# Kernel tuning notes

Hardware: AMD Instinct MI355X
Metric: run time of the kernel (lower is better)

The kernel has to match this reference:

```python
import jax, jax.numpy as jnp
import numpy as np
from jax import lax

_DN = ('NCHW', 'OIHW', 'NCHW')


def _box1(s, k):
    # Separable box sum (all-ones kxk kernel) on a single-channel map (B,1,H,W).
    pad = (k - 1) // 2
    kh = jnp.ones((1, 1, k, 1), s.dtype)
    kw = jnp.ones((1, 1, 1, k), s.dtype)
    y = lax.conv_general_dilated(s, kh, (1, 1), [(pad, pad), (0, 0)], dimension_numbers=_DN)
    return lax.conv_general_dilated(y, kw, (1, 1), [(0, 0), (pad, pad)], dimension_numbers=_DN)


def _cgf(x, y, k, eps):
    # ConvGuidedFilterDlicate with weight-1 Conv2d(C,C,k): every output channel of
    # box_filter(t) equals box_sum(t.sum(channels)), so we keep channel dim = 1 and broadcast.
    B, C, H, W = x.shape
    Nc = C * _box1(jnp.ones((1, 1, H, W), x.dtype), k)           # box_filter(ones(1,C,H,W))
    mean_x = _box1(x.sum(1, keepdims=True), k) / Nc              # (B,1,H,W)
    mean_y = _box1(y.sum(1, keepdims=True), k) / Nc
    cov_xy = _box1((x * y).sum(1, keepdims=True), k) / Nc - mean_x * mean_y
    var_x = _box1((x * x).sum(1, keepdims=True), k) / Nc - mean_x * mean_x
    A = cov_xy / (var_x + eps)
    b = mean_y - A * mean_x
    # torch's A/b have C identical channels; box_filter then sums them -> factor C.
    mean_A = C * _box1(A, k)
    mean_b = C * _box1(b, k)
    return mean_A * y + mean_b                                   # broadcasts to (B,C,H,W)


def setup_inputs() -> dict:
    key = jax.random.key(0)
    k1, k2 = jax.random.split(key)
    x_hr = jax.random.normal(k1, (16, 3, 512, 512), jnp.float32)
    w1 = jax.random.normal(k2, (3, 9), jnp.float32) * 0.1        # conv1 weight (O, 3*nin1)
    return {"x_hr": x_hr, "w1": w1}


def reference(x_hr, w1):
    F1 = _cgf(x_hr, x_hr, 3, 0.16)
    F2 = _cgf(F1, F1, 7, 0.04)
    F3 = _cgf(F2, F2, 15, 0.01)
    D = jnp.concatenate([x_hr - F1, F1 - F2, F2 - F3], axis=1)   # (B,9,H,W)
    return jnp.einsum('oi,bihw->bohw', w1, D)                    # 1x1 conv, no bias
```

## Files before the change

kernel.cpp:

```cpp
#include <hip/hip_runtime.h>

#define BB 16
#define CC 3
#define HH 512
#define WW 512
#define HWP (HH*WW)
#define NMAP ((size_t)BB*HWP)

template <int P, int CH, int MODE>
__global__ __launch_bounds__(512, (MODE == 3 ? 2 : 4))
void stage(const float* __restrict__ xin, const float2* __restrict__ sqin,
           float2* __restrict__ abo, float2* __restrict__ sqo,
           const float2* __restrict__ ab1, const float2* __restrict__ ab2,
           const float* __restrict__ w1, float* __restrict__ outp, float eps)
{
    constexpr int RD  = 2*P + 1;
    constexpr int LW  = 512 + 2*P;
    constexpr int NCH = HH / CH;
    __shared__ float2 eA[LW];
    __shared__ float2 eB[LW];

    const int t  = threadIdx.x;
    const int bx = blockIdx.x;
    const int b  = bx / NCH;
    const int h0 = (bx % NCH) * CH;
    const size_t mapbase = (size_t)b * HWP;
    const float*  xb  = (MODE != 2) ? (xin + (size_t)b * CC * HWP) : nullptr;
    const float2* sqb = (MODE != 1) ? (sqin + mapbase) : nullptr;

    if (t < 2*P) {
        int sl = (t < P) ? t : (512 + t);
        eA[sl] = make_float2(0.f, 0.f);
        eB[sl] = make_float2(0.f, 0.f);
    }

    const int w   = t;
    const int wlo = (w - P < 0) ? 0 : w - P;
    const int whi = (w + P > WW-1) ? WW-1 : w + P;
    const float rcw = 1.0f / (float)(whi - wlo + 1);

    float cs0 = 0.f, cs1 = 0.f;
    float ca  = 0.f, cb  = 0.f;
    float rA[RD], rB[RD];

    auto loadSQ = [&](int rr, float& sv, float& qv) {
        size_t o = (size_t)rr * WW + w;
        if constexpr (MODE == 1) {
            float x0 = xb[o], x1 = xb[o + HWP], x2 = xb[o + 2*HWP];
            sv = x0 + x1 + x2;
            qv = x0*x0 + x1*x1 + x2*x2;
        } else {
            float2 v = sqb[o];
            sv = v.x; qv = v.y;
        }
    };

    auto advance = [&](int r) {
        int rin = r + P, rout = r - P - 1;
        if (rin < HH)  { float sv, qv; loadSQ(rin,  sv, qv); cs0 += sv; cs1 += qv; }
        if (rout >= 0) { float sv, qv; loadSQ(rout, sv, qv); cs0 -= sv; cs1 -= qv; }
    };

    auto phase1 = [&](int r, float& Aout, float& Bout) {
        eA[t + P] = make_float2(cs0, cs1);
        __syncthreads();
        float hs0 = 0.f, hs1 = 0.f;
#pragma unroll
        for (int d = 0; d <= 2*P; ++d) { float2 v = eA[t + d]; hs0 += v.x; hs1 += v.y; }
        __syncthreads();
        int rlo = (r - P < 0) ? 0 : r - P;
        int rhi = (r + P > HH-1) ? HH-1 : r + P;
        float rNc  = (1.f/3.f) * rcw / (float)(rhi - rlo + 1);
        float mean = hs0 * rNc;
        float var  = hs1 * rNc - mean * mean;
        float A    = var / (var + eps);
        Aout = A;
        Bout = mean * (1.f - A);
    };

    float w1r[27];
    if constexpr (MODE == 3) {
#pragma unroll
        for (int k = 0; k < 27; ++k) w1r[k] = w1[k];
    }

#pragma unroll
    for (int d = 0; d <= 2*P; ++d) {
        int rr = h0 - 2*P + d;
        if (rr >= 0) { float sv, qv; loadSQ(rr, sv, qv); cs0 += sv; cs1 += qv; }
    }

#pragma unroll
    for (int j = 0; j < 2*P; ++j) {
        int r = h0 - P + j;
        if (j > 0) advance(r);
        float A = 0.f, Bv = 0.f;
        if (r >= 0) { phase1(r, A, Bv); ca += A; cb += Bv; }
        rA[j % RD] = A; rB[j % RD] = Bv;
    }

#pragma unroll
    for (int i = 0; i < CH; ++i) {
        int r = h0 + P + i;
        int h = h0 + i;
        advance(r);
        float A = 0.f, Bv = 0.f;
        if (r < HH) { phase1(r, A, Bv); ca += A; cb += Bv; }
        rA[(2*P + i) % RD] = A; rB[(2*P + i) % RD] = Bv;

        eB[t + P] = make_float2(ca, cb);
        __syncthreads();
        float sA = 0.f, sB = 0.f;
#pragma unroll
        for (int d = 0; d <= 2*P; ++d) { float2 v = eB[t + d]; sA += v.x; sB += v.y; }
        __syncthreads();

        size_t oi = mapbase + (size_t)h * WW + w;
        if constexpr (MODE != 3) {
            abo[oi] = make_float2(sA, sB);
            float sv, qv; loadSQ(h, sv, qv);
            float mA = 3.f * sA, mb = 3.f * sB;
            sqo[oi] = make_float2(mA*sv + 3.f*mb,
                                  mA*mA*qv + 2.f*mA*mb*sv + 3.f*mb*mb);
        } else {
            float a3 = 3.f*sA, b3 = 3.f*sB;
            float2 v1 = ab1[oi], v2 = ab2[oi];
            float a1 = 3.f*v1.x, b1 = 3.f*v1.y;
            float a2 = 3.f*v2.x, b2 = 3.f*v2.y;
            float P1 = a1,      Q1 = b1;
            float P2 = a2 * P1, Q2 = a2 * Q1 + b2;
            float P3 = a3 * P2, Q3 = a3 * Q2 + b3;
            float alpha[3] = {1.f - P1, P1 - P2, P2 - P3};
            float beta[3]  = {-Q1,      Q1 - Q2, Q2 - Q3};
            size_t xo = (size_t)h * WW + w;
            float xv0 = xb[xo], xv1 = xb[xo + HWP], xv2 = xb[xo + 2*HWP];
#pragma unroll
            for (int o = 0; o < 3; ++o) {
                float acc = 0.f;
#pragma unroll
                for (int g = 0; g < 3; ++g) {
                    float w0v = w1r[o*9 + g*3 + 0];
                    float wv1 = w1r[o*9 + g*3 + 1];
                    float w2v = w1r[o*9 + g*3 + 2];
                    acc += alpha[g] * (w0v*xv0 + wv1*xv1 + w2v*xv2)
                         + beta[g]  * (w0v + wv1 + w2v);
                }
                outp[(size_t)b * CC * HWP + (size_t)o * HWP + xo] = acc;
            }
        }
        ca -= rA[i % RD]; cb -= rB[i % RD];
    }
}

extern "C" void kernel_launch(void* const* d_in, const int* in_sizes, int n_in,
                              void* d_out, int out_size, void* d_ws, size_t ws_size,
                              hipStream_t stream) {
    (void)in_sizes; (void)n_in; (void)out_size; (void)ws_size;
    const float* x  = (const float*)d_in[0];
    const float* w1 = (const float*)d_in[1];
    float* out = (float*)d_out;

    float2* sq1 = (float2*)d_ws;
    float2* sq2 = sq1 + NMAP;
    float2* ab1 = sq2 + NMAP;
    float2* ab2 = ab1 + NMAP;

    dim3 bl(512);
    dim3 g(BB * (HH / 16));

    stage<1,16,1><<<g, bl, 0, stream>>>(x, nullptr, ab1, sq1,
                                        nullptr, nullptr, nullptr, nullptr, 0.16f);
    stage<3,16,2><<<g, bl, 0, stream>>>(nullptr, sq1, ab2, sq2,
                                        nullptr, nullptr, nullptr, nullptr, 0.04f);
    stage<7,16,3><<<g, bl, 0, stream>>>(x, sq2, nullptr, nullptr,
                                        ab1, ab2, w1, out, 0.01f);
}
```

Before: 220.7 us.

## Rewrite guided-filter stages with two-column threads and fused single-barrier row pipeline

```diff
diff --git a/kernel.cpp b/kernel.cpp
--- a/kernel.cpp
+++ b/kernel.cpp
@@ -1,154 +1,199 @@
 #include <hip/hip_runtime.h>
 
 #define BB 16
-#define CC 3
 #define HH 512
 #define WW 512
 #define HWP (HH*WW)
 #define NMAP ((size_t)BB*HWP)
 
+struct __align__(16) V4 { float x, y, z, w; };
+__device__ __forceinline__ V4 v4(float a, float b, float c, float d) { V4 r; r.x=a; r.y=b; r.z=c; r.w=d; return r; }
+__device__ __forceinline__ V4 v4z() { return v4(0.f,0.f,0.f,0.f); }
+__device__ __forceinline__ V4 vadd(V4 a, V4 b) { return v4(a.x+b.x, a.y+b.y, a.z+b.z, a.w+b.w); }
+__device__ __forceinline__ V4 vsub(V4 a, V4 b) { return v4(a.x-b.x, a.y-b.y, a.z-b.z, a.w-b.w); }
+
 template <int P, int CH, int MODE>
-__global__ __launch_bounds__(512, (MODE == 3 ? 2 : 4))
+__global__ __launch_bounds__(256, 2)
 void stage(const float* __restrict__ xin, const float2* __restrict__ sqin,
            float2* __restrict__ abo, float2* __restrict__ sqo,
-           const float2* __restrict__ ab1, const float2* __restrict__ ab2,
-           const float* __restrict__ w1, float* __restrict__ outp, float eps)
+           const float2* __restrict__ abp1, const float2* __restrict__ abp2,
+           const float* __restrict__ wt, float* __restrict__ outp, float eps)
 {
+    constexpr int PH  = (P - 1) / 2;
     constexpr int RD  = 2*P + 1;
-    constexpr int LW  = 512 + 2*P;
+    constexpr int NIT = CH + 2*P + 1;
     constexpr int NCH = HH / CH;
-    __shared__ float2 eA[LW];
-    __shared__ float2 eB[LW];
+    constexpr int NWG = BB * NCH;
+    constexpr int NPS = 256 + 2*PH;
+    constexpr int NEV = 257 + PH;
+    constexpr int NOD = 258 + PH;
+
+    __shared__ V4 PS[2][NPS];
+    __shared__ V4 EV[2][NEV];
+    __shared__ V4 OD[2][NOD];
 
     const int t  = threadIdx.x;
-    const int bx = blockIdx.x;
-    const int b  = bx / NCH;
-    const int h0 = (bx % NCH) * CH;
-    const size_t mapbase = (size_t)b * HWP;
-    const float*  xb  = (MODE != 2) ? (xin + (size_t)b * CC * HWP) : nullptr;
-    const float2* sqb = (MODE != 1) ? (sqin + mapbase) : nullptr;
-
-    if (t < 2*P) {
-        int sl = (t < P) ? t : (512 + t);
-        eA[sl] = make_float2(0.f, 0.f);
-        eB[sl] = make_float2(0.f, 0.f);
-    }
-
-    const int w   = t;
-    const int wlo = (w - P < 0) ? 0 : w - P;
-    const int whi = (w + P > WW-1) ? WW-1 : w + P;
-    const float rcw = 1.0f / (float)(whi - wlo + 1);
-
-    float cs0 = 0.f, cs1 = 0.f;
-    float ca  = 0.f, cb  = 0.f;
-    float rA[RD], rB[RD];
-
-    auto loadSQ = [&](int rr, float& sv, float& qv) {
-        size_t o = (size_t)rr * WW + w;
+    int bx = blockIdx.x;
+    int bid = (bx & 7) * (NWG / 8) + (bx >> 3);
+    const int b  = bid / NCH;
+    const int h0 = (bid % NCH) * CH;
+    const size_t mb_ = (size_t)b * HWP;
+    const float*  xb  = (MODE != 2) ? (xin + (size_t)b * 3 * HWP) : nullptr;
+    const float2* sqb = (MODE != 1) ? (sqin + mb_) : nullptr;
+
+    if (t < PH) {
+        PS[0][t] = v4z(); PS[1][t] = v4z();
+        PS[0][256+PH+t] = v4z(); PS[1][256+PH+t] = v4z();
+    }
+    if (t < PH + 1) {
+        OD[0][t] = v4z(); OD[1][t] = v4z();
+        EV[0][256+t] = v4z(); EV[1][256+t] = v4z();
+    }
+
+    const int c0 = 2*t, c1 = c0 + 1;
+    auto cwf = [&](int c) -> float {
+        int lo = c - P < 0 ? 0 : c - P, hi = c + P > WW-1 ? WW-1 : c + P;
+        return (float)(hi - lo + 1);
+    };
+    const float cw0 = cwf(c0), cw1 = cwf(c1);
+
+    auto loadrow = [&](int rr) -> V4 {
         if constexpr (MODE == 1) {
-            float x0 = xb[o], x1 = xb[o + HWP], x2 = xb[o + 2*HWP];
-            sv = x0 + x1 + x2;
-            qv = x0*x0 + x1*x1 + x2*x2;
+            size_t o = (size_t)rr * WW + c0;
+            float2 a0 = *(const float2*)(xb + o);
+            float2 a1 = *(const float2*)(xb + o + HWP);
+            float2 a2 = *(const float2*)(xb + o + 2*HWP);
+            return v4(a0.x+a1.x+a2.x, a0.x*a0.x + a1.x*a1.x + a2.x*a2.x,
+                      a0.y+a1.y+a2.y, a0.y*a0.y + a1.y*a1.y + a2.y*a2.y);
         } else {
-            float2 v = sqb[o];
-            sv = v.x; qv = v.y;
+            float4 v = ((const float4*)(sqb + (size_t)rr * WW))[t];
+            return v4(v.x, v.y, v.z, v.w);
         }
     };
 
-    auto advance = [&](int r) {
-        int rin = r + P, rout = r - P - 1;
-        if (rin < HH)  { float sv, qv; loadSQ(rin,  sv, qv); cs0 += sv; cs1 += qv; }
-        if (rout >= 0) { float sv, qv; loadSQ(rout, sv, qv); cs0 -= sv; cs1 -= qv; }
-    };
-
-    auto phase1 = [&](int r, float& Aout, float& Bout) {
-        eA[t + P] = make_float2(cs0, cs1);
-        __syncthreads();
-        float hs0 = 0.f, hs1 = 0.f;
-#pragma unroll
-        for (int d = 0; d <= 2*P; ++d) { float2 v = eA[t + d]; hs0 += v.x; hs1 += v.y; }
-        __syncthreads();
-        int rlo = (r - P < 0) ? 0 : r - P;
-        int rhi = (r + P > HH-1) ? HH-1 : r + P;
-        float rNc  = (1.f/3.f) * rcw / (float)(rhi - rlo + 1);
-        float mean = hs0 * rNc;
-        float var  = hs1 * rNc - mean * mean;
-        float A    = var / (var + eps);
-        Aout = A;
-        Bout = mean * (1.f - A);
-    };
+    V4 csv = v4z(), cav = v4z();
+    V4 rgv[RD];
+#pragma unroll
+    for (int i = 0; i < RD; ++i) rgv[i] = v4z();
+
+#pragma unroll
+    for (int d = 0; d <= 2*P; ++d) {
+        int rr = h0 - 2*P + d;
+        if (rr >= 0) csv = vadd(csv, loadrow(rr));
+    }
+    V4 nin = loadrow(h0 + 1);
 
     float w1r[27];
     if constexpr (MODE == 3) {
 #pragma unroll
-        for (int k = 0; k < 27; ++k) w1r[k] = w1[k];
-    }
-
-#pragma unroll
-    for (int d = 0; d <= 2*P; ++d) {
-        int rr = h0 - 2*P + d;
-        if (rr >= 0) { float sv, qv; loadSQ(rr, sv, qv); cs0 += sv; cs1 += qv; }
-    }
-
-#pragma unroll
-    for (int j = 0; j < 2*P; ++j) {
-        int r = h0 - P + j;
-        if (j > 0) advance(r);
-        float A = 0.f, Bv = 0.f;
-        if (r >= 0) { phase1(r, A, Bv); ca += A; cb += Bv; }
-        rA[j % RD] = A; rB[j % RD] = Bv;
-    }
-
-#pragma unroll
-    for (int i = 0; i < CH; ++i) {
-        int r = h0 + P + i;
-        int h = h0 + i;
-        advance(r);
-        float A = 0.f, Bv = 0.f;
-        if (r < HH) { phase1(r, A, Bv); ca += A; cb += Bv; }
-        rA[(2*P + i) % RD] = A; rB[(2*P + i) % RD] = Bv;
-
-        eB[t + P] = make_float2(ca, cb);
+        for (int k = 0; k < 27; ++k) w1r[k] = wt[k];
+    }
+    __syncthreads();
+
+#pragma unroll
+    for (int j = 0; j < NIT; ++j) {
+        const int r  = h0 - P + j;
+        const int bf = j & 1;
+        V4 e0 = v4(csv.x, csv.y, cav.x, cav.y);
+        V4 e1 = v4(csv.z, csv.w, cav.z, cav.w);
+        PS[bf][PH + t]     = vadd(e0, e1);
+        EV[bf][t]          = e0;
+        OD[bf][PH + 1 + t] = e1;
+
+        V4 nin2 = v4z(), outv = v4z();
+        if (j < NIT - 2) { int rr = r + 2 + P; if (rr < HH) nin2 = loadrow(rr); }
+        if (j < NIT - 1) { int rr = r - P;     if (rr >= 0) outv = loadrow(rr); }
+        const int h = r - P - 1;
+        V4 dv = v4z();
+        float4 q1v = make_float4(0,0,0,0), q2v = make_float4(0,0,0,0);
+        float2 xe0 = make_float2(0,0), xe1 = xe0, xe2 = xe0;
+        if (j >= 2*P + 1) {
+            if constexpr (MODE != 3) {
+                dv = loadrow(h);
+            } else {
+                size_t o = mb_ + (size_t)h * WW + c0;
+                q1v = *((const float4*)&abp1[o]);
+                q2v = *((const float4*)&abp2[o]);
+                size_t xo = (size_t)h * WW + c0;
+                xe0 = *(const float2*)(xb + xo);
+                xe1 = *(const float2*)(xb + xo + HWP);
+                xe2 = *(const float2*)(xb + xo + 2*HWP);
+            }
+        }
         __syncthreads();
-        float sA = 0.f, sB = 0.f;
-#pragma unroll
-        for (int d = 0; d <= 2*P; ++d) { float2 v = eB[t + d]; sA += v.x; sB += v.y; }
-        __syncthreads();
-
-        size_t oi = mapbase + (size_t)h * WW + w;
-        if constexpr (MODE != 3) {
-            abo[oi] = make_float2(sA, sB);
-            float sv, qv; loadSQ(h, sv, qv);
-            float mA = 3.f * sA, mb = 3.f * sB;
-            sqo[oi] = make_float2(mA*sv + 3.f*mb,
-                                  mA*mA*qv + 2.f*mA*mb*sv + 3.f*mb*mb);
-        } else {
-            float a3 = 3.f*sA, b3 = 3.f*sB;
-            float2 v1 = ab1[oi], v2 = ab2[oi];
-            float a1 = 3.f*v1.x, b1 = 3.f*v1.y;
-            float a2 = 3.f*v2.x, b2 = 3.f*v2.y;
-            float P1 = a1,      Q1 = b1;
-            float P2 = a2 * P1, Q2 = a2 * Q1 + b2;
-            float P3 = a3 * P2, Q3 = a3 * Q2 + b3;
-            float alpha[3] = {1.f - P1, P1 - P2, P2 - P3};
-            float beta[3]  = {-Q1,      Q1 - Q2, Q2 - Q3};
-            size_t xo = (size_t)h * WW + w;
-            float xv0 = xb[xo], xv1 = xb[xo + HWP], xv2 = xb[xo + 2*HWP];
-#pragma unroll
-            for (int o = 0; o < 3; ++o) {
-                float acc = 0.f;
-#pragma unroll
-                for (int g = 0; g < 3; ++g) {
-                    float w0v = w1r[o*9 + g*3 + 0];
-                    float wv1 = w1r[o*9 + g*3 + 1];
-                    float w2v = w1r[o*9 + g*3 + 2];
-                    acc += alpha[g] * (w0v*xv0 + wv1*xv1 + w2v*xv2)
-                         + beta[g]  * (w0v + wv1 + w2v);
+
+        V4 S = v4z();
+#pragma unroll
+        for (int i = -PH; i <= PH; ++i) S = vadd(S, PS[bf][PH + t + i]);
+        V4 W0 = vadd(S, OD[bf][t]);
+        V4 W1 = vadd(S, EV[bf][t + PH + 1]);
+
+        if (j >= 2*P + 1) {
+            if constexpr (MODE != 3) {
+                size_t o = mb_ + (size_t)h * WW + c0;
+                *((float4*)&abo[o]) = make_float4(W0.z, W0.w, W1.z, W1.w);
+                float mA0 = 3.f*W0.z, mb0 = 3.f*W0.w;
+                float mA1 = 3.f*W1.z, mb1 = 3.f*W1.w;
+                *((float4*)&sqo[o]) = make_float4(
+                    mA0*dv.x + 3.f*mb0,
+                    mA0*mA0*dv.y + 2.f*mA0*mb0*dv.x + 3.f*mb0*mb0,
+                    mA1*dv.z + 3.f*mb1,
+                    mA1*mA1*dv.w + 2.f*mA1*mb1*dv.z + 3.f*mb1*mb1);
+            } else {
+                float a3  = 3.f*W0.z, b3  = 3.f*W0.w;
+                float a3c = 3.f*W1.z, b3c = 3.f*W1.w;
+                float r0[3], r1[3];
+#pragma unroll
+                for (int c = 0; c < 2; ++c) {
+                    float P1 = 3.f * (c ? q1v.z : q1v.x), Q1 = 3.f * (c ? q1v.w : q1v.y);
+                    float a2 = 3.f * (c ? q2v.z : q2v.x), b2 = 3.f * (c ? q2v.w : q2v.y);
+                    float a3v = c ? a3c : a3,             b3v = c ? b3c : b3;
+                    float P2 = a2 * P1,  Q2 = a2 * Q1 + b2;
+                    float P3 = a3v * P2, Q3 = a3v * Q2 + b3v;
+                    float al[3] = {1.f - P1, P1 - P2, P2 - P3};
+                    float be[3] = {-Q1,      Q1 - Q2, Q2 - Q3};
+                    float x0 = c ? xe0.y : xe0.x;
+                    float x1 = c ? xe1.y : xe1.x;
+                    float x2 = c ? xe2.y : xe2.x;
+                    float* rr_ = c ? r1 : r0;
+#pragma unroll
+                    for (int oc = 0; oc < 3; ++oc) {
+                        float acc = 0.f;
+#pragma unroll
+                        for (int gg = 0; gg < 3; ++gg) {
+                            float wa = w1r[oc*9 + gg*3 + 0];
+                            float wb = w1r[oc*9 + gg*3 + 1];
+                            float wc = w1r[oc*9 + gg*3 + 2];
+                            acc += al[gg] * (wa*x0 + wb*x1 + wc*x2)
+                                 + be[gg] * (wa + wb + wc);
+                        }
+                        rr_[oc] = acc;
+                    }
                 }
-                outp[(size_t)b * CC * HWP + (size_t)o * HWP + xo] = acc;
+                float* ob = outp + (size_t)b * 3 * HWP + (size_t)h * WW + c0;
+#pragma unroll
+                for (int oc = 0; oc < 3; ++oc)
+                    *((float2*)(ob + (size_t)oc * HWP)) = make_float2(r0[oc], r1[oc]);
             }
         }
-        ca -= rA[i % RD]; cb -= rB[i % RD];
+
+        if (j < NIT - 1) {
+            V4 Av = v4z();
+            if ((unsigned)r < (unsigned)HH) {
+                int lo = r-P < 0 ? 0 : r-P, hi = r+P > HH-1 ? HH-1 : r+P;
+                float chh = (float)(hi - lo + 1);
+                float rn0 = 1.f/(3.f*chh*cw0), rn1 = 1.f/(3.f*chh*cw1);
+                float m0 = W0.x*rn0, m1 = W1.x*rn1;
+                float v0 = W0.y*rn0 - m0*m0, v1 = W1.y*rn1 - m1*m1;
+                float a0 = v0/(v0 + eps), a1 = v1/(v1 + eps);
+                Av = v4(a0, m0*(1.f-a0), a1, m1*(1.f-a1));
+            }
+            const int ri = j % RD;
+            cav = vadd(cav, vsub(Av, rgv[ri]));
+            rgv[ri] = Av;
+            csv = vadd(csv, vsub(nin, outv));
+            nin = nin2;
+        }
     }
 }
 
@@ -165,13 +210,12 @@
     float2* ab1 = sq2 + NMAP;
     float2* ab2 = ab1 + NMAP;
 
-    dim3 bl(512);
-    dim3 g(BB * (HH / 16));
-
-    stage<1,16,1><<<g, bl, 0, stream>>>(x, nullptr, ab1, sq1,
+    dim3 bl(256);
+
+    stage<1,4,1><<<dim3(BB*(HH/4)), bl, 0, stream>>>(x, nullptr, ab1, sq1,
                                         nullptr, nullptr, nullptr, nullptr, 0.16f);
-    stage<3,16,2><<<g, bl, 0, stream>>>(nullptr, sq1, ab2, sq2,
+    stage<3,8,2><<<dim3(BB*(HH/8)), bl, 0, stream>>>(nullptr, sq1, ab2, sq2,
                                         nullptr, nullptr, nullptr, nullptr, 0.04f);
-    stage<7,16,3><<<g, bl, 0, stream>>>(x, sq2, nullptr, nullptr,
+    stage<7,8,3><<<dim3(BB*(HH/8)), bl, 0, stream>>>(x, sq2, nullptr, nullptr,
                                         ab1, ab2, w1, out, 0.01f);
 }
```

After: 203.8 us. 7.7% less time.
